# Kernel tuning notes

Measured on AMD Instinct MI355X. Metric: run time of the kernel, lower is better.

## Reference

```python
import jax, jax.numpy as jnp
import numpy as np

NUM_POSITIONS = 4096
EMBED_DIM = 512
BSZ, SEQ_LEN = 16, 4096


def setup_inputs() -> dict:
    key = jax.random.key(0)
    k1, k2 = jax.random.split(key)
    input_tensor = jax.random.normal(k1, (BSZ, SEQ_LEN, EMBED_DIM), dtype=jnp.float32)
    pv = jax.random.normal(k2, (NUM_POSITIONS, EMBED_DIM), dtype=jnp.float32)
    # L2-normalize each position vector (as in _init_position_vectors)
    pv = pv / jnp.linalg.norm(pv, axis=1, keepdims=True)
    return {"input_tensor": input_tensor, "position_vectors": pv}


def reference(input_tensor, position_vectors):
    # input_tensor: [B, S, D]; position_vectors: [P, D] with S <= P.
    seq_len, d = input_tensor.shape[1], input_tensor.shape[-1]
    pos = position_vectors[:seq_len]  # [S, D]
    # Batched circular convolution over the last axis via rFFT.
    x_fft = jnp.fft.rfft(input_tensor, axis=-1)          # [B, S, D//2+1] complex
    p_fft = jnp.fft.rfft(pos, axis=-1)[None, :, :]       # [1, S, D//2+1]
    out = jnp.fft.irfft(x_fft * p_fft, n=d, axis=-1)     # [B, S, D]
    return out.astype(input_tensor.dtype)
```

## Files before the change

### kernel.cpp

```cpp
#include <hip/hip_runtime.h>
#include <math.h>

#ifndef M_PI
#define M_PI 3.14159265358979323846
#endif

#define SEQ 4096
#define DIM 512

#define REG_SZ 656

__device__ __forceinline__ void wsync(){
  asm volatile("s_waitcnt lgkmcnt(0)" ::: "memory");
  __builtin_amdgcn_wave_barrier();
}

__device__ __forceinline__ float2 cadd(float2 a, float2 b){ return make_float2(a.x+b.x, a.y+b.y); }
__device__ __forceinline__ float2 csub(float2 a, float2 b){ return make_float2(a.x-b.x, a.y-b.y); }
__device__ __forceinline__ float2 cmul(float2 a, float2 b){
  return make_float2(fmaf(a.x, b.x, -(a.y*b.y)), fmaf(a.x, b.y, a.y*b.x));
}
__device__ __forceinline__ float2 cmulc(float2 a, float2 b){
  return make_float2(fmaf(a.x, b.x, a.y*b.y), fmaf(a.y, b.x, -(a.x*b.y)));
}
__device__ __forceinline__ float2 mul_mi(float2 a){ return make_float2(a.y, -a.x); }

__device__ __forceinline__ void dft8(const float2* in, float2* out){
  float2 t0 = cadd(in[0], in[4]), t1 = csub(in[0], in[4]);
  float2 t2 = cadd(in[2], in[6]), t3 = csub(in[2], in[6]);
  float2 E0 = cadd(t0, t2), E2 = csub(t0, t2);
  float2 m3 = mul_mi(t3);
  float2 E1 = cadd(t1, m3), E3 = csub(t1, m3);
  float2 s0 = cadd(in[1], in[5]), s1 = csub(in[1], in[5]);
  float2 s2 = cadd(in[3], in[7]), s3 = csub(in[3], in[7]);
  float2 O0 = cadd(s0, s2), O2 = csub(s0, s2);
  float2 n3 = mul_mi(s3);
  float2 O1 = cadd(s1, n3), O3 = csub(s1, n3);
  const float C = 0.70710678118654752440f;
  float2 w1o = make_float2(C*(O1.x + O1.y), C*(O1.y - O1.x));
  float2 w2o = mul_mi(O2);
  float2 w3o = make_float2(C*(O3.y - O3.x), -(C*(O3.x + O3.y)));
  out[0] = cadd(E0, O0); out[4] = csub(E0, O0);
  out[1] = cadd(E1, w1o); out[5] = csub(E1, w1o);
  out[2] = cadd(E2, w2o); out[6] = csub(E2, w2o);
  out[3] = cadd(E3, w3o); out[7] = csub(E3, w3o);
}

__device__ __forceinline__ void idft8(const float2* in, float2* out){
  float2 t[8];
  dft8(in, t);
  out[0]=t[0]; out[1]=t[7]; out[2]=t[6]; out[3]=t[5];
  out[4]=t[4]; out[5]=t[3]; out[6]=t[2]; out[7]=t[1];
}

__device__ __forceinline__ void make_twiddles(int lane, float2* wA, float2* wB){
  const int b = lane & 7;
  float sv, cv;
  sincosf(-2.0f*(float)M_PI*(float)lane*(1.0f/512.0f), &sv, &cv);
  const float2 a1 = make_float2(cv, sv);
  sincosf(-2.0f*(float)M_PI*(float)b*(1.0f/64.0f), &sv, &cv);
  const float2 b1 = make_float2(cv, sv);
  wA[0] = make_float2(1.f, 0.f); wB[0] = make_float2(1.f, 0.f);
  wA[1] = a1; wB[1] = b1;
  #pragma unroll
  for (int r = 2; r < 8; ++r){ wA[r] = cmul(wA[r-1], a1); wB[r] = cmul(wB[r-1], b1); }
}

__device__ __forceinline__ void fft512_fwd(float2* v, float2* lds, int lane,
                                           const float2* wA, const float2* wB){
  const int a = lane >> 3, b = lane & 7;
  float2 t[8];
  dft8(v, t);
  #pragma unroll
  for (int r = 1; r < 8; ++r) t[r] = cmul(t[r], wA[r]);
  wsync();
  #pragma unroll
  for (int r = 0; r < 8; ++r) lds[72*r + lane] = t[r];
  wsync();
  #pragma unroll
  for (int j2 = 0; j2 < 8; ++j2) v[j2] = lds[72*a + b + 8*j2];
  dft8(v, t);
  #pragma unroll
  for (int r2 = 1; r2 < 8; ++r2) t[r2] = cmul(t[r2], wB[r2]);
  wsync();
  #pragma unroll
  for (int r2 = 0; r2 < 8; ++r2) lds[a + 82*r2 + 10*b] = t[r2];
  wsync();
  #pragma unroll
  for (int i2 = 0; i2 < 8; ++i2) v[i2] = lds[a + 82*b + 10*i2];
  dft8(v, t);
  #pragma unroll
  for (int m = 0; m < 8; ++m) v[m] = t[m];
}

__device__ __forceinline__ void fft512_inv(float2* v, float2* lds, int lane,
                                           const float2* wA, const float2* wB){
  const int a = lane >> 3, b = lane & 7;
  float2 t[8];
  idft8(v, t);
  wsync();
  #pragma unroll
  for (int i2 = 0; i2 < 8; ++i2) lds[a + 82*b + 10*i2] = t[i2];
  wsync();
  #pragma unroll
  for (int r2 = 0; r2 < 8; ++r2) v[r2] = lds[a + 82*r2 + 10*b];
  #pragma unroll
  for (int r2 = 1; r2 < 8; ++r2) v[r2] = cmulc(v[r2], wB[r2]);
  idft8(v, t);
  wsync();
  #pragma unroll
  for (int j2 = 0; j2 < 8; ++j2) lds[72*a + b + 8*j2] = t[j2];
  wsync();
  #pragma unroll
  for (int r = 0; r < 8; ++r) v[r] = lds[72*r + lane];
  #pragma unroll
  for (int r = 1; r < 8; ++r) v[r] = cmulc(v[r], wA[r]);
  idft8(v, t);
  #pragma unroll
  for (int j = 0; j < 8; ++j) v[j] = t[j];
}

__global__ void __launch_bounds__(256)
pfft_kernel(const float* __restrict__ p, float2* __restrict__ pspec){
  __shared__ float2 lds_all[4 * REG_SZ];
  const int lane = threadIdx.x & 63;
  const int wid  = threadIdx.x >> 6;
  float2* lds = lds_all + wid * REG_SZ;
  const int s = blockIdx.x * 4 + wid;

  float2 wA[8], wB[8];
  make_twiddles(lane, wA, wB);

  const float* prow = p + (size_t)s * DIM;
  float2 pf[8];
  #pragma unroll
  for (int j = 0; j < 8; ++j) pf[j] = make_float2(prow[lane + 64*j], 0.f);
  fft512_fwd(pf, lds, lane, wA, wB);
  #pragma unroll
  for (int m = 0; m < 8; ++m){
    pf[m].x *= (1.0f/512.0f); pf[m].y *= (1.0f/512.0f);
    pspec[(size_t)s * DIM + 64*m + lane] = pf[m];
  }
}

__global__ void __launch_bounds__(256)
circconv_kernel(const float* __restrict__ x, const float2* __restrict__ pspec,
                float* __restrict__ out){
  __shared__ float2 lds_all[4 * REG_SZ];
  const int lane = threadIdx.x & 63;
  const int wid  = threadIdx.x >> 6;
  float2* lds = lds_all + wid * REG_SZ;

  const int g    = blockIdx.x * 4 + wid;
  const int s    = g >> 3;
  const int pr   = g & 7;

  const size_t row_stride = (size_t)SEQ * DIM;
  const size_t base0 = ((size_t)(2*pr) * SEQ + s) * DIM;
  const size_t base1 = base0 + row_stride;

  float2 pf[8];
  #pragma unroll
  for (int m = 0; m < 8; ++m) pf[m] = pspec[(size_t)s * DIM + 64*m + lane];

  float re[8], im[8];
  #pragma unroll
  for (int j = 0; j < 8; ++j){
    re[j] = x[base0 + lane + 64*j];
    im[j] = x[base1 + lane + 64*j];
  }

  float2 wA[8], wB[8];
  make_twiddles(lane, wA, wB);

  float2 v[8];
  #pragma unroll
  for (int j = 0; j < 8; ++j) v[j] = make_float2(re[j], im[j]);

  fft512_fwd(v, lds, lane, wA, wB);
  #pragma unroll
  for (int m = 0; m < 8; ++m) v[m] = cmul(v[m], pf[m]);
  fft512_inv(v, lds, lane, wA, wB);

  #pragma unroll
  for (int j = 0; j < 8; ++j){
    out[base0 + lane + 64*j] = v[j].x;
    out[base1 + lane + 64*j] = v[j].y;
  }
}

__global__ void __launch_bounds__(256)
circconv_fallback_kernel(const float* __restrict__ x, const float* __restrict__ p,
                         float* __restrict__ out){
  __shared__ float2 lds_all[4 * REG_SZ];
  const int lane = threadIdx.x & 63;
  const int wid  = threadIdx.x >> 6;
  float2* lds = lds_all + wid * REG_SZ;

  const int g    = blockIdx.x * 4 + wid;
  const int s    = g >> 1;
  const int half = g & 1;

  float2 wA[8], wB[8];
  make_twiddles(lane, wA, wB);

  float2 pf[8];
  {
    const float* prow = p + (size_t)s * DIM;
    #pragma unroll
    for (int j = 0; j < 8; ++j) pf[j] = make_float2(prow[lane + 64*j], 0.f);
    fft512_fwd(pf, lds, lane, wA, wB);
    #pragma unroll
    for (int m = 0; m < 8; ++m){ pf[m].x *= (1.0f/512.0f); pf[m].y *= (1.0f/512.0f); }
  }

  const size_t row_stride = (size_t)SEQ * DIM;
  const int b_lo = half * 8;
  for (int bb = b_lo; bb < b_lo + 8; bb += 2){
    const size_t base0 = ((size_t)bb * SEQ + s) * DIM;
    const size_t base1 = base0 + row_stride;
    float2 v[8];
    #pragma unroll
    for (int j = 0; j < 8; ++j)
      v[j] = make_float2(x[base0 + lane + 64*j], x[base1 + lane + 64*j]);
    fft512_fwd(v, lds, lane, wA, wB);
    #pragma unroll
    for (int m = 0; m < 8; ++m) v[m] = cmul(v[m], pf[m]);
    fft512_inv(v, lds, lane, wA, wB);
    #pragma unroll
    for (int j = 0; j < 8; ++j){
      out[base0 + lane + 64*j] = v[j].x;
      out[base1 + lane + 64*j] = v[j].y;
    }
  }
}

extern "C" void kernel_launch(void* const* d_in, const int* in_sizes, int n_in,
                              void* d_out, int out_size, void* d_ws, size_t ws_size,
                              hipStream_t stream) {
  (void)in_sizes; (void)n_in; (void)out_size;
  const float* x  = (const float*)d_in[0];
  const float* p  = (const float*)d_in[1];
  float* o        = (float*)d_out;

  const size_t pspec_bytes = (size_t)SEQ * DIM * sizeof(float2);
  if (ws_size >= pspec_bytes){
    float2* pspec = (float2*)d_ws;
    pfft_kernel<<<SEQ/4, 256, 0, stream>>>(p, pspec);
    circconv_kernel<<<SEQ*8/4, 256, 0, stream>>>(x, pspec, o);
  } else {
    circconv_fallback_kernel<<<SEQ*2/4, 256, 0, stream>>>(x, p, o);
  }
}
```

Baseline: 247.0 us.

## Make circconv persistent with register prefetch of next item and fewer LDS syncs

The circular-convolution kernel becomes a persistent-style loop: 8192 waves each handle four row-pairs and prefetch the next item's input into registers while the current FFT runs. Blocks shrink to 128 threads. Redundant wave syncs before LDS writes are removed, and the second-stage LDS stride changes from 82 to 78, shrinking per-wave scratch. The aim is to hide global load latency and cut sync overhead. The cost is extra register pressure, and dropping the pre-write syncs relies on in-order LDS access within a wave.

```diff
diff --git a/kernel.cpp b/kernel.cpp
--- a/kernel.cpp
+++ b/kernel.cpp
@@ -8,7 +8,11 @@
 #define SEQ 4096
 #define DIM 512
 
-#define REG_SZ 656
+#define REG_SZ 624
+
+#define TOTAL_ITEMS (SEQ*8)
+#define NW 8192
+#define ITERS (TOTAL_ITEMS/NW)
 
 __device__ __forceinline__ void wsync(){
   asm volatile("s_waitcnt lgkmcnt(0)" ::: "memory");
@@ -73,7 +77,6 @@
   dft8(v, t);
   #pragma unroll
   for (int r = 1; r < 8; ++r) t[r] = cmul(t[r], wA[r]);
-  wsync();
   #pragma unroll
   for (int r = 0; r < 8; ++r) lds[72*r + lane] = t[r];
   wsync();
@@ -82,12 +85,11 @@
   dft8(v, t);
   #pragma unroll
   for (int r2 = 1; r2 < 8; ++r2) t[r2] = cmul(t[r2], wB[r2]);
-  wsync();
-  #pragma unroll
-  for (int r2 = 0; r2 < 8; ++r2) lds[a + 82*r2 + 10*b] = t[r2];
-  wsync();
-  #pragma unroll
-  for (int i2 = 0; i2 < 8; ++i2) v[i2] = lds[a + 82*b + 10*i2];
+  #pragma unroll
+  for (int r2 = 0; r2 < 8; ++r2) lds[a + 78*r2 + 10*b] = t[r2];
+  wsync();
+  #pragma unroll
+  for (int i2 = 0; i2 < 8; ++i2) v[i2] = lds[a + 78*b + 10*i2];
   dft8(v, t);
   #pragma unroll
   for (int m = 0; m < 8; ++m) v[m] = t[m];
@@ -98,16 +100,14 @@
   const int a = lane >> 3, b = lane & 7;
   float2 t[8];
   idft8(v, t);
-  wsync();
-  #pragma unroll
-  for (int i2 = 0; i2 < 8; ++i2) lds[a + 82*b + 10*i2] = t[i2];
-  wsync();
-  #pragma unroll
-  for (int r2 = 0; r2 < 8; ++r2) v[r2] = lds[a + 82*r2 + 10*b];
+  #pragma unroll
+  for (int i2 = 0; i2 < 8; ++i2) lds[a + 78*b + 10*i2] = t[i2];
+  wsync();
+  #pragma unroll
+  for (int r2 = 0; r2 < 8; ++r2) v[r2] = lds[a + 78*r2 + 10*b];
   #pragma unroll
   for (int r2 = 1; r2 < 8; ++r2) v[r2] = cmulc(v[r2], wB[r2]);
   idft8(v, t);
-  wsync();
   #pragma unroll
   for (int j2 = 0; j2 < 8; ++j2) lds[72*a + b + 8*j2] = t[j2];
   wsync();
@@ -143,49 +143,65 @@
   }
 }
 
-__global__ void __launch_bounds__(256)
+__global__ void __launch_bounds__(128)
 circconv_kernel(const float* __restrict__ x, const float2* __restrict__ pspec,
                 float* __restrict__ out){
-  __shared__ float2 lds_all[4 * REG_SZ];
+  __shared__ float2 lds_all[2 * REG_SZ];
   const int lane = threadIdx.x & 63;
   const int wid  = threadIdx.x >> 6;
   float2* lds = lds_all + wid * REG_SZ;
 
-  const int g    = blockIdx.x * 4 + wid;
-  const int s    = g >> 3;
-  const int pr   = g & 7;
-
+  const int wg = blockIdx.x * 2 + wid;
   const size_t row_stride = (size_t)SEQ * DIM;
-  const size_t base0 = ((size_t)(2*pr) * SEQ + s) * DIM;
-  const size_t base1 = base0 + row_stride;
-
-  float2 pf[8];
-  #pragma unroll
-  for (int m = 0; m < 8; ++m) pf[m] = pspec[(size_t)s * DIM + 64*m + lane];
-
-  float re[8], im[8];
-  #pragma unroll
-  for (int j = 0; j < 8; ++j){
-    re[j] = x[base0 + lane + 64*j];
-    im[j] = x[base1 + lane + 64*j];
-  }
 
   float2 wA[8], wB[8];
   make_twiddles(lane, wA, wB);
 
-  float2 v[8];
-  #pragma unroll
-  for (int j = 0; j < 8; ++j) v[j] = make_float2(re[j], im[j]);
-
-  fft512_fwd(v, lds, lane, wA, wB);
-  #pragma unroll
-  for (int m = 0; m < 8; ++m) v[m] = cmul(v[m], pf[m]);
-  fft512_inv(v, lds, lane, wA, wB);
-
+  int item = wg;
+  size_t b0 = ((size_t)(2*(item & 7)) * SEQ + (item >> 3)) * DIM;
+  size_t b1 = b0 + row_stride;
+  float pre0[8], pre1[8];
   #pragma unroll
   for (int j = 0; j < 8; ++j){
-    out[base0 + lane + 64*j] = v[j].x;
-    out[base1 + lane + 64*j] = v[j].y;
+    pre0[j] = x[b0 + lane + 64*j];
+    pre1[j] = x[b1 + lane + 64*j];
+  }
+
+  #pragma unroll 1
+  for (int it = 0; it < ITERS; ++it){
+    const int s = item >> 3;
+    const size_t cb0 = b0, cb1 = b1;
+
+    float2 v[8];
+    #pragma unroll
+    for (int j = 0; j < 8; ++j) v[j] = make_float2(pre0[j], pre1[j]);
+
+    float2 pf[8];
+    #pragma unroll
+    for (int m = 0; m < 8; ++m) pf[m] = pspec[(size_t)s * DIM + 64*m + lane];
+
+    if (it + 1 < ITERS){
+      const int ni = item + NW;
+      b0 = ((size_t)(2*(ni & 7)) * SEQ + (ni >> 3)) * DIM;
+      b1 = b0 + row_stride;
+      #pragma unroll
+      for (int j = 0; j < 8; ++j){
+        pre0[j] = x[b0 + lane + 64*j];
+        pre1[j] = x[b1 + lane + 64*j];
+      }
+      item = ni;
+    }
+
+    fft512_fwd(v, lds, lane, wA, wB);
+    #pragma unroll
+    for (int m = 0; m < 8; ++m) v[m] = cmul(v[m], pf[m]);
+    fft512_inv(v, lds, lane, wA, wB);
+
+    #pragma unroll
+    for (int j = 0; j < 8; ++j){
+      out[cb0 + lane + 64*j] = v[j].x;
+      out[cb1 + lane + 64*j] = v[j].y;
+    }
   }
 }
 
@@ -247,7 +263,7 @@
   if (ws_size >= pspec_bytes){
     float2* pspec = (float2*)d_ws;
     pfft_kernel<<<SEQ/4, 256, 0, stream>>>(p, pspec);
-    circconv_kernel<<<SEQ*8/4, 256, 0, stream>>>(x, pspec, o);
+    circconv_kernel<<<NW/2, 128, 0, stream>>>(x, pspec, o);
   } else {
     circconv_fallback_kernel<<<SEQ*2/4, 256, 0, stream>>>(x, p, o);
   }
```

Result: no change. 250.4 us (+1.4%).
